# Optimization experiments

Measured on AMD Instinct MI355X. Metric: run time of the kernel, lower is better.

## Reference

```python
import jax, jax.numpy as jnp
import numpy as np
from jax import lax

H, W, K, B = 64, 64, 64, 64
OFFSETS = [(0, 1), (2, 1), (1, 0), (1, 2)]  # up, down, left, right slices into padded grid


def setup_inputs() -> dict:
    key = jax.random.key(0)
    ks = jax.random.split(key, 7)
    n = H * W * 3
    s = lambda d: 1.0 / np.sqrt(d)
    return {
        "obs_flat": jax.random.normal(ks[0], (B, n), jnp.float32),
        "phi_w": jax.random.normal(ks[1], (n, n), jnp.float32) * s(n),
        "phi_b": jax.random.normal(ks[2], (n,), jnp.float32) * s(n),
        "w1": jax.random.normal(ks[3], (36, 16), jnp.float32) * s(36),
        "b1": jax.random.normal(ks[4], (16,), jnp.float32) * s(36),
        "w2": jax.random.normal(ks[5], (16, 4), jnp.float32) * s(16),
        "b2": jax.random.normal(ks[6], (4,), jnp.float32) * s(16),
    }


def _vin(rin, rout, p):
    # rin, rout, p: [B, H, W]. K Bellman-style 4-neighbor sweeps.
    prin = jnp.pad(rin, ((0, 0), (1, 1), (1, 1)))
    rin_sh = jnp.stack([prin[:, ho:ho + H, wo:wo + W] for ho, wo in OFFSETS])  # [4,B,H,W]
    rout_masked = rout[None] * (rin_sh != 0).astype(rin.dtype)                 # [4,B,H,W]

    def step(V, _):
        pv = jnp.pad(V, ((0, 0), (1, 1), (1, 1)))
        v_sh = jnp.stack([pv[:, ho:ho + H, wo:wo + W] for ho, wo in OFFSETS])
        nv = p[None] * v_sh + rin_sh - rout_masked
        return jnp.maximum(V, nv.max(axis=0)), None

    V0 = jnp.zeros_like(rin)
    V, _ = lax.scan(step, V0, None, length=K)
    return V


def reference(obs_flat, phi_w, phi_b, w1, b1, w2, b2):
    obs = obs_flat.reshape(B, H, W, 3)
    phi = (obs_flat @ phi_w + phi_b).reshape(B, H, W, 3)
    rin, rout = phi[..., 0], phi[..., 1]
    p = jax.nn.softmax(phi[..., 2].reshape(B, H * W), axis=1).reshape(B, H, W)

    V = _vin(rin, rout, p)  # [B,H,W]
    obs_val = jnp.concatenate([obs, V[..., None]], axis=-1)  # [B,H,W,4]
    padded = jnp.pad(obs_val, ((0, 0), (1, 1), (1, 1), (0, 0)))

    # agent position = location of the (one-hot) nonzero in channel 1
    flat = jnp.argmax(obs[..., 1].reshape(B, -1), axis=1)
    pi, pj = flat // W, flat % W
    patch = jax.vmap(lambda x, i, j: lax.dynamic_slice(x, (i, j, 0), (3, 3, 4)))(padded, pi, pj)

    h = jax.nn.relu(patch.reshape(B, 36) @ w1 + b1)
    logit = h @ w2 + b2  # [B, 4]
    return logit
```

## Files before the change

kernel.cpp:

```cpp
#include <hip/hip_runtime.h>
#include <hip/hip_bf16.h>

typedef __attribute__((ext_vector_type(8))) short short8;
typedef __attribute__((ext_vector_type(4))) float floatx4;
typedef __attribute__((ext_vector_type(4))) unsigned short ushort4v;
typedef __attribute__((ext_vector_type(8))) unsigned short ushort8v;

#define N_DIM 12288
#define SPLITK 4
#define KCHUNK (N_DIM / SPLITK)
#define KSTEP 64
#define NTILE 64

__device__ __forceinline__ unsigned short f2bf(float f) {
  union { float f; unsigned int i; } x; x.f = f;
  unsigned int r = x.i + 0x7fffu + ((x.i >> 16) & 1u);
  return (unsigned short)(r >> 16);
}

__global__ __launch_bounds__(256) void gemm_phi(
    const float* __restrict__ obs, const float* __restrict__ W,
    const float* __restrict__ bias, float* __restrict__ phi)
{
  __shared__ unsigned short A_s[64 * 72];
  __shared__ unsigned short W_s[64 * 72];

  const int t = threadIdx.x;
  const int n0 = blockIdx.x * NTILE;
  const int s  = blockIdx.y;
  const int k0 = s * KCHUNK;
  const int lane = t & 63, wv = t >> 6;
  const int l16 = lane & 15, q = lane >> 4;
  const int m0f = 16 * wv;

  floatx4 acc[4];
#pragma unroll
  for (int i = 0; i < 4; i++) acc[i] = (floatx4){0.f, 0.f, 0.f, 0.f};

  const int am = t >> 2, akq = (t & 3) * 16;
  const int rg = t >> 4, cg = t & 15;

  for (int it = 0; it < KCHUNK / KSTEP; ++it) {
    const int kb = k0 + it * KSTEP;
    {
      const float* src = obs + (size_t)am * N_DIM + kb + akq;
      floatx4 f0 = *(const floatx4*)(src);
      floatx4 f1 = *(const floatx4*)(src + 4);
      floatx4 f2 = *(const floatx4*)(src + 8);
      floatx4 f3 = *(const floatx4*)(src + 12);
      ushort8v u0, u1;
#pragma unroll
      for (int i = 0; i < 4; i++) {
        u0[i] = f2bf(f0[i]); u0[4 + i] = f2bf(f1[i]);
        u1[i] = f2bf(f2[i]); u1[4 + i] = f2bf(f3[i]);
      }
      *(ushort8v*)&A_s[am * 72 + akq]     = u0;
      *(ushort8v*)&A_s[am * 72 + akq + 8] = u1;
    }
    {
      const size_t base = (size_t)(kb + 4 * rg) * N_DIM + (n0 + 4 * cg);
      floatx4 r0 = *(const floatx4*)(W + base);
      floatx4 r1 = *(const floatx4*)(W + base + N_DIM);
      floatx4 r2 = *(const floatx4*)(W + base + 2 * N_DIM);
      floatx4 r3 = *(const floatx4*)(W + base + 3 * N_DIM);
#pragma unroll
      for (int i = 0; i < 4; i++) {
        ushort4v v = { f2bf(r0[i]), f2bf(r1[i]), f2bf(r2[i]), f2bf(r3[i]) };
        *(ushort4v*)&W_s[(4 * cg + i) * 72 + 4 * rg] = v;
      }
    }
    __syncthreads();
#pragma unroll
    for (int kk = 0; kk < 2; ++kk) {
      short8 af = *(const short8*)&A_s[(m0f + l16) * 72 + 32 * kk + 8 * q];
#pragma unroll
      for (int nt = 0; nt < 4; ++nt) {
        short8 wf = *(const short8*)&W_s[(16 * nt + l16) * 72 + 32 * kk + 8 * q];
        acc[nt] = __builtin_amdgcn_mfma_f32_16x16x32_bf16(af, wf, acc[nt], 0, 0, 0);
      }
    }
    __syncthreads();
  }
#pragma unroll
  for (int nt = 0; nt < 4; ++nt) {
    const int ncol = n0 + 16 * nt + l16;
    const float bv = (s == 0) ? bias[ncol] : 0.f;
#pragma unroll
    for (int r = 0; r < 4; ++r) {
      const int m = m0f + q * 4 + r;
      atomicAdd(&phi[(size_t)m * N_DIM + ncol], acc[nt][r] + bv);
    }
  }
}

#define VSTR 76
#define VOFF(h, w) (((h) + 1) * VSTR + (w) + 4)

__global__ __launch_bounds__(256) void vin_mlp(
    const float* __restrict__ obs, const float* __restrict__ phi,
    const float* __restrict__ w1, const float* __restrict__ b1,
    const float* __restrict__ w2, const float* __restrict__ b2,
    float* __restrict__ out)
{
  __shared__ float Vb[2][66 * VSTR];
  __shared__ float red_v[256];
  __shared__ int   red_i[256];

  const int b = blockIdx.x;
  const int t = threadIdx.x;
  const int ty = t >> 4, tx = t & 15;
  const int h0 = ty * 4, w0 = tx * 4;

  for (int i = t; i < 2 * 66 * VSTR; i += 256) (&Vb[0][0])[i] = 0.f;

  float rin[16], rout[16], lg[16];
#pragma unroll
  for (int r = 0; r < 4; r++) {
    const int j = 3 * ((h0 + r) * 64 + w0);
    const floatx4* p4 = (const floatx4*)(phi + (size_t)b * N_DIM + j);
    floatx4 x0 = p4[0], x1 = p4[1], x2 = p4[2];
    float f[12];
#pragma unroll
    for (int c = 0; c < 4; c++) { f[c] = x0[c]; f[4 + c] = x1[c]; f[8 + c] = x2[c]; }
#pragma unroll
    for (int c = 0; c < 4; c++) {
      rin [r * 4 + c] = f[3 * c + 0];
      rout[r * 4 + c] = f[3 * c + 1];
      lg  [r * 4 + c] = f[3 * c + 2];
    }
  }

  float lmax = -3.4e38f;
#pragma unroll
  for (int i = 0; i < 16; i++) lmax = fmaxf(lmax, lg[i]);
  __syncthreads();
  red_v[t] = lmax; __syncthreads();
  for (int o = 128; o > 0; o >>= 1) { if (t < o) red_v[t] = fmaxf(red_v[t], red_v[t + o]); __syncthreads(); }
  const float M = red_v[0];
  __syncthreads();
  float p[16]; float esum = 0.f;
#pragma unroll
  for (int i = 0; i < 16; i++) { p[i] = __expf(lg[i] - M); esum += p[i]; }
  red_v[t] = esum; __syncthreads();
  for (int o = 128; o > 0; o >>= 1) { if (t < o) red_v[t] += red_v[t + o]; __syncthreads(); }
  const float inv = 1.f / red_v[0];
  __syncthreads();
#pragma unroll
  for (int i = 0; i < 16; i++) p[i] *= inv;

#pragma unroll
  for (int r = 0; r < 4; r++) {
    floatx4 rr = { rin[r * 4 + 0], rin[r * 4 + 1], rin[r * 4 + 2], rin[r * 4 + 3] };
    *(floatx4*)&Vb[1][VOFF(h0 + r, w0)] = rr;
  }
  __syncthreads();
  float cu[16], cdn[16], cl[16], cr[16];
#pragma unroll
  for (int r = 0; r < 4; r++) {
#pragma unroll
    for (int c = 0; c < 4; c++) {
      const int i = r * 4 + c, h = h0 + r, w = w0 + c;
      const float nu = Vb[1][VOFF(h - 1, w)];
      const float nd = Vb[1][VOFF(h + 1, w)];
      const float nl = Vb[1][VOFF(h, w - 1)];
      const float nr = Vb[1][VOFF(h, w + 1)];
      cu [i] = nu - (nu != 0.f ? rout[i] : 0.f);
      cdn[i] = nd - (nd != 0.f ? rout[i] : 0.f);
      cl [i] = nl - (nl != 0.f ? rout[i] : 0.f);
      cr [i] = nr - (nr != 0.f ? rout[i] : 0.f);
    }
  }
  __syncthreads();

  float v[16];
#pragma unroll
  for (int i = 0; i < 16; i++) v[i] = 0.f;

  for (int k = 0; k < 64; k++) {
    const float* Vc = Vb[k & 1];
    float* Vn = Vb[(k & 1) ^ 1];
    const floatx4 top = *(const floatx4*)&Vc[VOFF(h0 - 1, w0)];
    const floatx4 bot = *(const floatx4*)&Vc[VOFF(h0 + 4, w0)];
    float lf[4], rt[4];
#pragma unroll
    for (int r = 0; r < 4; r++) { lf[r] = Vc[VOFF(h0 + r, w0 - 1)]; rt[r] = Vc[VOFF(h0 + r, w0 + 4)]; }
    float nv[16];
#pragma unroll
    for (int r = 0; r < 4; r++) {
#pragma unroll
      for (int c = 0; c < 4; c++) {
        const int i = r * 4 + c;
        const float vu = (r == 0) ? top[c] : v[i - 4];
        const float vd = (r == 3) ? bot[c] : v[i + 4];
        const float vl = (c == 0) ? lf[r] : v[i - 1];
        const float vr = (c == 3) ? rt[r] : v[i + 1];
        const float m1 = fmaxf(fmaf(p[i], vu, cu[i]), fmaf(p[i], vd, cdn[i]));
        const float m2 = fmaxf(fmaf(p[i], vl, cl[i]), fmaf(p[i], vr, cr[i]));
        nv[i] = fmaxf(v[i], fmaxf(m1, m2));
      }
    }
#pragma unroll
    for (int r = 0; r < 4; r++) {
      floatx4 w4 = { nv[r * 4 + 0], nv[r * 4 + 1], nv[r * 4 + 2], nv[r * 4 + 3] };
      *(floatx4*)&Vn[VOFF(h0 + r, w0)] = w4;
    }
#pragma unroll
    for (int i = 0; i < 16; i++) v[i] = nv[i];
    __syncthreads();
  }

  float amax = -3.4e38f; int aidx = 0;
#pragma unroll
  for (int r = 0; r < 4; r++) {
#pragma unroll
    for (int c = 0; c < 4; c++) {
      const int cell = (h0 + r) * 64 + (w0 + c);
      const float val = obs[(size_t)b * N_DIM + 3 * cell + 1];
      if (val > amax) { amax = val; aidx = cell; }
    }
  }
  red_v[t] = amax; red_i[t] = aidx;
  __syncthreads();
  for (int o = 128; o > 0; o >>= 1) {
    if (t < o) {
      const float v2 = red_v[t + o]; const int i2 = red_i[t + o];
      if (v2 > red_v[t] || (v2 == red_v[t] && i2 < red_i[t])) { red_v[t] = v2; red_i[t] = i2; }
    }
    __syncthreads();
  }
  const int pos = red_i[0];
  const int pi = pos >> 6, pj = pos & 63;
  __syncthreads();

  if (t < 36) {
    const int di = t / 12, rem = t % 12, dj = rem / 4, c4 = rem & 3;
    const int hh = pi - 1 + di, ww = pj - 1 + dj;
    float pv;
    if (c4 < 3) {
      pv = (hh >= 0 && hh < 64 && ww >= 0 && ww < 64)
           ? obs[(size_t)b * N_DIM + 3 * (hh * 64 + ww) + c4] : 0.f;
    } else {
      pv = Vb[0][VOFF(hh, ww)];
    }
    red_v[t] = pv;
  }
  __syncthreads();
  if (t < 16) {
    float a = b1[t];
#pragma unroll
    for (int j = 0; j < 36; j++) a = fmaf(red_v[j], w1[j * 16 + t], a);
    red_v[64 + t] = fmaxf(a, 0.f);
  }
  __syncthreads();
  if (t < 4) {
    float a = b2[t];
#pragma unroll
    for (int i = 0; i < 16; i++) a = fmaf(red_v[64 + i], w2[i * 4 + t], a);
    out[b * 4 + t] = a;
  }
}

extern "C" void kernel_launch(void* const* d_in, const int* in_sizes, int n_in,
                              void* d_out, int out_size, void* d_ws, size_t ws_size,
                              hipStream_t stream)
{
  (void)in_sizes; (void)n_in; (void)out_size; (void)ws_size;
  const float* obs  = (const float*)d_in[0];
  const float* phiw = (const float*)d_in[1];
  const float* phib = (const float*)d_in[2];
  const float* w1   = (const float*)d_in[3];
  const float* b1   = (const float*)d_in[4];
  const float* w2   = (const float*)d_in[5];
  const float* b2   = (const float*)d_in[6];
  float* phi = (float*)d_ws;
  float* out = (float*)d_out;

  hipMemsetAsync(phi, 0, (size_t)64 * N_DIM * sizeof(float), stream);
  hipLaunchKernelGGL(gemm_phi, dim3(N_DIM / NTILE, SPLITK), dim3(256), 0, stream,
                     obs, phiw, phib, phi);
  hipLaunchKernelGGL(vin_mlp, dim3(64), dim3(256), 0, stream,
                     obs, phi, w1, b1, w2, b2, out);
}
```

Measured before the change: 833.3 us.

## Double-buffer GEMM tiles with register prefetch and replace atomics with split-K partials

The phi GEMM now double-buffers its LDS tiles and prefetches the next K tile into registers before computing on the current one, which drops one barrier per iteration and overlaps global loads with MFMA work. Split-K results are written to separate partial buffers instead of atomicAdd into a zeroed buffer, so the memset is removed. The VIN kernel sums the four partials when it loads phi. This trades atomic traffic for extra workspace and extra reads in the second kernel, and relies on the workspace being large enough for four partial copies.

```diff
diff --git a/kernel.cpp b/kernel.cpp
--- a/kernel.cpp
+++ b/kernel.cpp
@@ -10,6 +10,7 @@
 #define SPLITK 4
 #define KCHUNK (N_DIM / SPLITK)
 #define KSTEP 64
+#define KITERS (KCHUNK / KSTEP)
 #define NTILE 64
 
 __device__ __forceinline__ unsigned short f2bf(float f) {
@@ -20,10 +21,10 @@
 
 __global__ __launch_bounds__(256) void gemm_phi(
     const float* __restrict__ obs, const float* __restrict__ W,
-    const float* __restrict__ bias, float* __restrict__ phi)
+    const float* __restrict__ bias, float* __restrict__ phi_part)
 {
-  __shared__ unsigned short A_s[64 * 72];
-  __shared__ unsigned short W_s[64 * 72];
+  __shared__ unsigned short A_s[2][64 * 72];
+  __shared__ unsigned short W_s[2][64 * 72];
 
   const int t = threadIdx.x;
   const int n0 = blockIdx.x * NTILE;
@@ -33,54 +34,61 @@
   const int l16 = lane & 15, q = lane >> 4;
   const int m0f = 16 * wv;
 
-  floatx4 acc[4];
-#pragma unroll
-  for (int i = 0; i < 4; i++) acc[i] = (floatx4){0.f, 0.f, 0.f, 0.f};
-
   const int am = t >> 2, akq = (t & 3) * 16;
   const int rg = t >> 4, cg = t & 15;
 
-  for (int it = 0; it < KCHUNK / KSTEP; ++it) {
-    const int kb = k0 + it * KSTEP;
+  const float* aptr = obs + (size_t)am * N_DIM + k0 + akq;
+  const float* wptr = W + (size_t)(k0 + 4 * rg) * N_DIM + (n0 + 4 * cg);
+
+  floatx4 fa0, fa1, fa2, fa3, fw0, fw1, fw2, fw3;
+#define LOAD_TILE(ap, wp) do {                                              \
+    fa0 = *(const floatx4*)(ap);      fa1 = *(const floatx4*)((ap) + 4);    \
+    fa2 = *(const floatx4*)((ap) + 8); fa3 = *(const floatx4*)((ap) + 12);  \
+    fw0 = *(const floatx4*)(wp);              fw1 = *(const floatx4*)((wp) + N_DIM); \
+    fw2 = *(const floatx4*)((wp) + 2 * N_DIM); fw3 = *(const floatx4*)((wp) + 3 * N_DIM); \
+  } while (0)
+
+  LOAD_TILE(aptr, wptr);
+
+  floatx4 acc[4];
+#pragma unroll
+  for (int i = 0; i < 4; i++) acc[i] = (floatx4){0.f, 0.f, 0.f, 0.f};
+
+  for (int it = 0; it < KITERS; ++it) {
+    const int cur = it & 1;
     {
-      const float* src = obs + (size_t)am * N_DIM + kb + akq;
-      floatx4 f0 = *(const floatx4*)(src);
-      floatx4 f1 = *(const floatx4*)(src + 4);
-      floatx4 f2 = *(const floatx4*)(src + 8);
-      floatx4 f3 = *(const floatx4*)(src + 12);
       ushort8v u0, u1;
 #pragma unroll
       for (int i = 0; i < 4; i++) {
-        u0[i] = f2bf(f0[i]); u0[4 + i] = f2bf(f1[i]);
-        u1[i] = f2bf(f2[i]); u1[4 + i] = f2bf(f3[i]);
+        u0[i] = f2bf(fa0[i]); u0[4 + i] = f2bf(fa1[i]);
+        u1[i] = f2bf(fa2[i]); u1[4 + i] = f2bf(fa3[i]);
       }
-      *(ushort8v*)&A_s[am * 72 + akq]     = u0;
-      *(ushort8v*)&A_s[am * 72 + akq + 8] = u1;
-    }
-    {
-      const size_t base = (size_t)(kb + 4 * rg) * N_DIM + (n0 + 4 * cg);
-      floatx4 r0 = *(const floatx4*)(W + base);
-      floatx4 r1 = *(const floatx4*)(W + base + N_DIM);
-      floatx4 r2 = *(const floatx4*)(W + base + 2 * N_DIM);
-      floatx4 r3 = *(const floatx4*)(W + base + 3 * N_DIM);
+      *(ushort8v*)&A_s[cur][am * 72 + akq]     = u0;
+      *(ushort8v*)&A_s[cur][am * 72 + akq + 8] = u1;
 #pragma unroll
       for (int i = 0; i < 4; i++) {
-        ushort4v v = { f2bf(r0[i]), f2bf(r1[i]), f2bf(r2[i]), f2bf(r3[i]) };
-        *(ushort4v*)&W_s[(4 * cg + i) * 72 + 4 * rg] = v;
+        ushort4v v = { f2bf(fw0[i]), f2bf(fw1[i]), f2bf(fw2[i]), f2bf(fw3[i]) };
+        *(ushort4v*)&W_s[cur][(4 * cg + i) * 72 + 4 * rg] = v;
       }
     }
+    if (it + 1 < KITERS) {
+      const float* ap = aptr + (it + 1) * KSTEP;
+      const float* wp = wptr + (size_t)(it + 1) * KSTEP * N_DIM;
+      LOAD_TILE(ap, wp);
+    }
     __syncthreads();
 #pragma unroll
     for (int kk = 0; kk < 2; ++kk) {
-      short8 af = *(const short8*)&A_s[(m0f + l16) * 72 + 32 * kk + 8 * q];
+      short8 af = *(const short8*)&A_s[cur][(m0f + l16) * 72 + 32 * kk + 8 * q];
 #pragma unroll
       for (int nt = 0; nt < 4; ++nt) {
-        short8 wf = *(const short8*)&W_s[(16 * nt + l16) * 72 + 32 * kk + 8 * q];
+        short8 wf = *(const short8*)&W_s[cur][(16 * nt + l16) * 72 + 32 * kk + 8 * q];
         acc[nt] = __builtin_amdgcn_mfma_f32_16x16x32_bf16(af, wf, acc[nt], 0, 0, 0);
       }
     }
-    __syncthreads();
-  }
+  }
+
+  float* dst = phi_part + (size_t)s * 64 * N_DIM;
 #pragma unroll
   for (int nt = 0; nt < 4; ++nt) {
     const int ncol = n0 + 16 * nt + l16;
@@ -88,9 +96,10 @@
 #pragma unroll
     for (int r = 0; r < 4; ++r) {
       const int m = m0f + q * 4 + r;
-      atomicAdd(&phi[(size_t)m * N_DIM + ncol], acc[nt][r] + bv);
-    }
-  }
+      dst[(size_t)m * N_DIM + ncol] = acc[nt][r] + bv;
+    }
+  }
+#undef LOAD_TILE
 }
 
 #define VSTR 76
@@ -117,8 +126,17 @@
 #pragma unroll
   for (int r = 0; r < 4; r++) {
     const int j = 3 * ((h0 + r) * 64 + w0);
-    const floatx4* p4 = (const floatx4*)(phi + (size_t)b * N_DIM + j);
-    floatx4 x0 = p4[0], x1 = p4[1], x2 = p4[2];
+    const float* base = phi + (size_t)b * N_DIM + j;
+    floatx4 x0 = *(const floatx4*)(base);
+    floatx4 x1 = *(const floatx4*)(base + 4);
+    floatx4 x2 = *(const floatx4*)(base + 8);
+#pragma unroll
+    for (int sp = 1; sp < SPLITK; sp++) {
+      const float* bs = base + (size_t)sp * 64 * N_DIM;
+      x0 += *(const floatx4*)(bs);
+      x1 += *(const floatx4*)(bs + 4);
+      x2 += *(const floatx4*)(bs + 8);
+    }
     float f[12];
 #pragma unroll
     for (int c = 0; c < 4; c++) { f[c] = x0[c]; f[4 + c] = x1[c]; f[8 + c] = x2[c]; }
@@ -275,7 +293,6 @@
   float* phi = (float*)d_ws;
   float* out = (float*)d_out;
 
-  hipMemsetAsync(phi, 0, (size_t)64 * N_DIM * sizeof(float), stream);
   hipLaunchKernelGGL(gemm_phi, dim3(N_DIM / NTILE, SPLITK), dim3(256), 0, stream,
                      obs, phiw, phib, phi);
   hipLaunchKernelGGL(vin_mlp, dim3(64), dim3(256), 0, stream,
```

Measured after the change: 819.0 us. About the same (-1.7%).
